# Optimization experiments

Measured on AMD Instinct MI355X. Metric: run time of the kernel, lower is better.

Reference implementation:

```python
import jax, jax.numpy as jnp
import numpy as np

B, S, E, H = 2, 2048, 1024, 16
D = E // H  # d_k = n_wires = 64


def setup_inputs() -> dict:
    key = jax.random.key(0)
    ks = jax.random.split(key, 6)
    x = jax.random.normal(ks[0], (B, S, E), dtype=jnp.float32)
    scale = 0.02
    Wq = jax.random.normal(ks[1], (E, E), dtype=jnp.float32) * scale
    Wk = jax.random.normal(ks[2], (E, E), dtype=jnp.float32) * scale
    Wv = jax.random.normal(ks[3], (E, E), dtype=jnp.float32) * scale
    Wc = jax.random.normal(ks[4], (E, E), dtype=jnp.float32) * scale
    bc = jnp.zeros((E,), dtype=jnp.float32)
    return {"x": x, "Wq": Wq, "Wk": Wk, "Wv": Wv, "Wc": Wc, "bc": bc}


def _split_heads(t):
    # [B,S,E] -> [B,H,S,D]
    return t.reshape(B, S, H, D).transpose(0, 2, 1, 3)


def _quantum(t):
    # RX(theta_i) per wire + CNOT ladder + per-wire PauliZ expectation:
    # <Z_j> = prod_{i<=j} cos(theta_i)  (closed form of the circuit)
    return jnp.cumprod(jnp.cos(t), axis=-1)


def reference(x, Wq, Wk, Wv, Wc, bc):
    q = _quantum(_split_heads(x @ Wq.T))  # [B,H,S,D]
    k = _quantum(_split_heads(x @ Wk.T))
    v = _quantum(_split_heads(x @ Wv.T))
    scores = jnp.einsum('bhsd,bhtd->bhst', q, k) / jnp.sqrt(jnp.float32(D))
    attn = jax.nn.softmax(scores, axis=-1)
    out = jnp.einsum('bhst,bhtd->bhsd', attn, v)  # [B,H,S,D]
    out = out.transpose(0, 2, 1, 3).reshape(B, S, E)
    return out @ Wc.T + bc
```

## Files before the change

### kernel.cpp

```cpp
#include <hip/hip_runtime.h>
#include <hip/hip_bf16.h>

constexpr int Bc = 2, Sc = 2048, Ec = 1024, Hc = 16, Dc = 64;
constexpr int Mrows = Bc * Sc;
constexpr int Kdim  = Ec;

#define QSCALE 0.18033688011112042f

typedef float  floatx4 __attribute__((ext_vector_type(4)));
typedef short  shortx8 __attribute__((ext_vector_type(8)));

__device__ __forceinline__ unsigned int pack2bf(float a, float b) {
    union { float f; unsigned int u; } ca, cb;
    ca.f = a; cb.f = b;
    return ((ca.u + 0x8000u) >> 16) | ((cb.u + 0x8000u) & 0xffff0000u);
}
__device__ inline float bf2f(unsigned short u) {
    union { unsigned int i; float f; } c; c.i = ((unsigned int)u) << 16; return c.f;
}
__device__ inline float exp2_fast(float x) {
#if __has_builtin(__builtin_amdgcn_exp2f)
    return __builtin_amdgcn_exp2f(x);
#else
    return __expf(x * 0.69314718056f);
#endif
}

__device__ __forceinline__ void gll16(const void* g, void* lds) {
    __builtin_amdgcn_global_load_lds(
        (const __attribute__((address_space(1))) void*)g,
        (__attribute__((address_space(3))) void*)lds, 16, 0, 0);
}

__global__ __launch_bounds__(256) void convert_all_kernel(
    const float* __restrict__ x,  const float* __restrict__ Wq,
    const float* __restrict__ Wk, const float* __restrict__ Wv,
    const float* __restrict__ Wc,
    unsigned short* __restrict__ xb,  unsigned short* __restrict__ Wqb,
    unsigned short* __restrict__ Wkb, unsigned short* __restrict__ Wvb,
    unsigned short* __restrict__ Wcb)
{
    const long t = (long)blockIdx.x * 256 + threadIdx.x;
    const long i = t * 4;
    const float* src; unsigned short* dst; long off;
    if (i < 4194304) { src = x; dst = xb; off = i; }
    else {
        long j = i - 4194304;
        int wsel = (int)(j >> 20);
        off = j & 1048575;
        src = (wsel == 0) ? Wq : (wsel == 1) ? Wk : (wsel == 2) ? Wv : Wc;
        dst = (wsel == 0) ? Wqb : (wsel == 1) ? Wkb : (wsel == 2) ? Wvb : Wcb;
    }
    float4 v = *(const float4*)(src + off);
    uint2 u;
    u.x = pack2bf(v.x, v.y);
    u.y = pack2bf(v.z, v.w);
    *(uint2*)(dst + off) = u;
}

__global__ __launch_bounds__(256) void proj_mfma_kernel(
    const unsigned short* __restrict__ Ab,
    const unsigned short* __restrict__ Wqb,
    const unsigned short* __restrict__ Wkb,
    const unsigned short* __restrict__ Wvb,
    unsigned short* __restrict__ oq,
    unsigned short* __restrict__ ok,
    unsigned short* __restrict__ ov)
{
    __shared__ __align__(16) char smem[33792];
    float (*Cs)[132] = (float(*)[132])smem;
    __shared__ float Sp[64][9];

    const int z = blockIdx.z;
    const unsigned short* Wb = (z == 0) ? Wqb : (z == 1) ? Wkb : Wvb;
    unsigned short* out      = (z == 0) ? oq  : (z == 1) ? ok  : ov;
    const int mode = (z == 2) ? 1 : 0;
    const float osc = (z == 0) ? QSCALE : 1.0f;

    const int tid = threadIdx.x;
    const int lane = tid & 63;
    const int w = tid >> 6, l15 = tid & 15, quad = (tid >> 4) & 3;
    const int wq = w >> 1, wn = w & 1;
    const int m0 = blockIdx.x * 128;
    const int n0 = blockIdx.y * 128;
    const int h0 = n0 >> 6;
    const int sw = l15 & 7;

    floatx4 acc[4][4];
    #pragma unroll
    for (int ms = 0; ms < 4; ++ms)
        #pragma unroll
        for (int ns = 0; ns < 4; ++ns)
            #pragma unroll
            for (int e = 0; e < 4; ++e) acc[ms][ns][e] = 0.0f;

    for (int k0 = 0; k0 < Kdim; k0 += 64) {
        #pragma unroll
        for (int j = 0; j < 4; ++j) {
            int idx = j * 64 + lane;
            int row = 32 * w + (idx >> 3);
            int cg  = ((idx & 7) ^ (idx >> 3)) & 7;
            gll16(Ab + (size_t)(m0 + row) * Kdim + k0 + cg * 8,
                  smem + 4096 * w + 1024 * j);
            gll16(Wb + (size_t)(n0 + row) * Kdim + k0 + cg * 8,
                  smem + 16384 + 4096 * w + 1024 * j);
        }
        __syncthreads();
        #pragma unroll
        for (int ks = 0; ks < 2; ++ks) {
            shortx8 af[4], bf[4];
            #pragma unroll
            for (int ms = 0; ms < 4; ++ms)
                af[ms] = *(shortx8*)(smem + (64 * wq + 16 * ms + l15) * 128
                                     + (((4 * ks + quad) ^ sw) << 4));
            #pragma unroll
            for (int ns = 0; ns < 4; ++ns)
                bf[ns] = *(shortx8*)(smem + 16384 + (64 * wn + 16 * ns + l15) * 128
                                     + (((4 * ks + quad) ^ sw) << 4));
            #pragma unroll
            for (int ms = 0; ms < 4; ++ms)
                #pragma unroll
                for (int ns = 0; ns < 4; ++ns)
                    acc[ms][ns] = __builtin_amdgcn_mfma_f32_16x16x32_bf16(
                        af[ms], bf[ns], acc[ms][ns], 0, 0, 0);
        }
        __syncthreads();
    }

    const int b = m0 >> 11;
    const int sbase = m0 & (Sc - 1);

    for (int pass = 0; pass < 2; ++pass) {
        if (wq == pass) {
            #pragma unroll
            for (int ms = 0; ms < 4; ++ms)
                #pragma unroll
                for (int ns = 0; ns < 4; ++ns)
                    #pragma unroll
                    for (int r = 0; r < 4; ++r)
                        Cs[16 * ms + 4 * quad + r][64 * wn + 16 * ns + l15] =
                            __cosf(acc[ms][ns][r]);
        }
        __syncthreads();
        #pragma unroll
        for (int t = tid; t < 512; t += 256) {
            int row = t >> 3, seg = t & 7;
            float pr = 1.0f;
            #pragma unroll
            for (int c = 0; c < 16; ++c) pr *= Cs[row][seg * 16 + c];
            Sp[row][seg] = pr;
        }
        __syncthreads();
        if (mode == 0) {
            #pragma unroll
            for (int t = tid; t < 512; t += 256) {
                int row = t >> 3, seg = t & 7;
                float p = 1.0f;
                for (int j = (seg & 4); j < seg; ++j) p *= Sp[row][j];
                unsigned int dw[8];
                #pragma unroll
                for (int c2 = 0; c2 < 8; ++c2) {
                    p *= Cs[row][seg * 16 + 2 * c2];     float a = p * osc;
                    p *= Cs[row][seg * 16 + 2 * c2 + 1]; float bb = p * osc;
                    dw[c2] = pack2bf(a, bb);
                }
                int h = h0 + (seg >> 2);
                int s = sbase + pass * 64 + row;
                size_t base = (((size_t)b * Hc + h) * Sc + s) * Dc + (seg & 3) * 16;
                *(uint4*)(out + base)     = *(uint4*)&dw[0];
                *(uint4*)(out + base + 8) = *(uint4*)&dw[4];
            }
            __syncthreads();
        } else {
            #pragma unroll
            for (int t = tid; t < 512; t += 256) {
                int row = t >> 3, seg = t & 7;
                float p = 1.0f;
                for (int j = (seg & 4); j < seg; ++j) p *= Sp[row][j];
                #pragma unroll
                for (int c = 0; c < 16; ++c) { p *= Cs[row][seg * 16 + c]; Cs[row][seg * 16 + c] = p; }
            }
            __syncthreads();
            #pragma unroll
            for (int t = tid; t < 512; t += 256) {
                int col = t >> 2, chunk = t & 3;
                int h = h0 + (col >> 6), d = col & 63;
                unsigned int dw[8];
                #pragma unroll
                for (int j2 = 0; j2 < 8; ++j2)
                    dw[j2] = pack2bf(Cs[chunk * 16 + 2 * j2][col],
                                     Cs[chunk * 16 + 2 * j2 + 1][col]);
                size_t base = (((size_t)b * Hc + h) * Dc + d) * Sc
                              + sbase + pass * 64 + chunk * 16;
                *(uint4*)(out + base)     = *(uint4*)&dw[0];
                *(uint4*)(out + base + 8) = *(uint4*)&dw[4];
            }
            __syncthreads();
        }
    }
}

__global__ __launch_bounds__(256) void attn_mfma_kernel(
    const unsigned short* __restrict__ qg,
    const unsigned short* __restrict__ kg,
    const unsigned short* __restrict__ vtg,
    unsigned short* __restrict__ o1,
    unsigned short* __restrict__ o2,
    float* __restrict__ lpart)
{
    __shared__ __align__(16) unsigned short Ks[2][32][64];
    __shared__ __align__(16) unsigned short VTs[2][64][32];
    __shared__ __align__(16) unsigned short Pq[64][72];

    const int tid  = threadIdx.x;
    const int lane = tid & 63;
    const int w    = tid >> 6;
    const int l15  = tid & 15;
    const int quad = (tid >> 4) & 3;
    const int qb   = blockIdx.x;
    const int half = blockIdx.y;
    const int bh   = blockIdx.z;
    const int sw   = l15 & 7;

    const unsigned short* qp = qg  + (size_t)bh * Sc * Dc;
    const unsigned short* kp = kg  + (size_t)bh * Sc * Dc;
    const unsigned short* vp = vtg + (size_t)bh * Dc * Sc;

    int qrow[2];
    shortx8 qf[2][2];
    #pragma unroll
    for (int qs = 0; qs < 2; ++qs) {
        qrow[qs] = qb * 128 + 32 * w + 16 * qs + l15;
        qf[qs][0] = *(const shortx8*)(qp + (size_t)qrow[qs] * Dc + 8 * quad);
        qf[qs][1] = *(const shortx8*)(qp + (size_t)qrow[qs] * Dc + 32 + 8 * quad);
    }

    floatx4 Oacc[2][4];
    #pragma unroll
    for (int qs = 0; qs < 2; ++qs)
        #pragma unroll
        for (int mt = 0; mt < 4; ++mt)
            #pragma unroll
            for (int e = 0; e < 4; ++e) Oacc[qs][mt][e] = 0.0f;
    float lsum[2] = {0.0f, 0.0f};

    const unsigned short* kgl = kp
        + (size_t)(half * 1024 + 8 * w + (lane >> 3)) * Dc
        + (((lane & 7) ^ ((lane >> 3) & 7)) * 8);
    const unsigned short* vgl = vp
        + (size_t)(16 * w + (lane >> 2)) * Sc + half * 1024 + (lane & 3) * 8;

    gll16(kgl, &Ks[0][8 * w][0]);
    gll16(vgl, &VTs[0][16 * w][0]);

    for (int it = 0; it < 32; ++it) {
        const int buf = it & 1;
        __syncthreads();
        if (it + 1 < 32) {
            const int nb = (it + 1) & 1;
            gll16(kgl + (size_t)(it + 1) * 32 * Dc, &Ks[nb][8 * w][0]);
            gll16(vgl + (it + 1) * 32,              &VTs[nb][16 * w][0]);
        }

        shortx8 kf[2][2], vf[4];
        #pragma unroll
        for (int ks = 0; ks < 2; ++ks)
            #pragma unroll
            for (int mtp = 0; mtp < 2; ++mtp)
                kf[ks][mtp] = *(shortx8*)&Ks[buf][16 * mtp + l15]
                                            [(((4 * ks + quad) ^ sw) & 7) * 8];
        #pragma unroll
        for (int mt = 0; mt < 4; ++mt)
            vf[mt] = *(shortx8*)&VTs[buf][16 * mt + l15][8 * quad];

        #pragma unroll
        for (int qs = 0; qs < 2; ++qs) {
            floatx4 st[2];
            #pragma unroll
            for (int mtp = 0; mtp < 2; ++mtp)
                #pragma unroll
                for (int e = 0; e < 4; ++e) st[mtp][e] = 0.0f;
            #pragma unroll
            for (int ks = 0; ks < 2; ++ks)
                #pragma unroll
                for (int mtp = 0; mtp < 2; ++mtp)
                    st[mtp] = __builtin_amdgcn_mfma_f32_16x16x32_bf16(
                        kf[ks][mtp], qf[qs][ks], st[mtp], 0, 0, 0);

            float rs = 0.0f;
            #pragma unroll
            for (int mtp = 0; mtp < 2; ++mtp) {
                float p0 = exp2_fast(st[mtp][0]);
                float p1 = exp2_fast(st[mtp][1]);
                float p2 = exp2_fast(st[mtp][2]);
                float p3 = exp2_fast(st[mtp][3]);
                rs += (p0 + p1) + (p2 + p3);
                uint2 u;
                u.x = pack2bf(p0, p1);
                u.y = pack2bf(p2, p3);
                *(uint2*)&Pq[16 * w + l15][16 * mtp + 4 * quad] = u;
            }
            lsum[qs] += rs;

            shortx8 pf = *(shortx8*)&Pq[16 * w + l15][8 * quad];
            #pragma unroll
            for (int mt = 0; mt < 4; ++mt)
                Oacc[qs][mt] = __builtin_amdgcn_mfma_f32_16x16x32_bf16(
                    vf[mt], pf, Oacc[qs][mt], 0, 0, 0);
        }
    }

    const int b = bh >> 4, hh = bh & 15;
    unsigned short* opart = half ? o2 : o1;
    float* lp = lpart + ((size_t)half * (Bc * Hc) + bh) * Sc;
    #pragma unroll
    for (int qs = 0; qs < 2; ++qs) {
        float l = lsum[qs];
        l += __shfl_xor(l, 16, 64);
        l += __shfl_xor(l, 32, 64);
        if (quad == 0) lp[qrow[qs]] = l;
        #pragma unroll
        for (int mt = 0; mt < 4; ++mt) {
            uint2 u;
            u.x = pack2bf(Oacc[qs][mt][0], Oacc[qs][mt][1]);
            u.y = pack2bf(Oacc[qs][mt][2], Oacc[qs][mt][3]);
            size_t base = ((size_t)b * Sc + qrow[qs]) * Ec + hh * 64 + 16 * mt + 4 * quad;
            *(uint2*)(opart + base) = u;
        }
    }
}

__global__ __launch_bounds__(256) void combine_kernel(
    unsigned short* __restrict__ o1,
    const unsigned short* __restrict__ o2,
    const float* __restrict__ lpart)
{
    const size_t t = (size_t)blockIdx.x * 256 + threadIdx.x;
    const size_t base = t * 8;
    const int e = (int)(base & (Ec - 1));
    const int h = e >> 6;
    const size_t bs = base >> 10;
    const int b = (int)(bs >> 11), s = (int)(bs & (Sc - 1));
    const int bh = b * Hc + h;
    const float l = lpart[(size_t)bh * Sc + s]
                  + lpart[(size_t)(Bc * Hc + bh) * Sc + s];
    const float inv = 1.0f / l;
    uint4 a = *(const uint4*)(o1 + base);
    uint4 c = *(const uint4*)(o2 + base);
    const unsigned short* ua = (const unsigned short*)&a;
    const unsigned short* uc = (const unsigned short*)&c;
    unsigned int dw[4];
    #pragma unroll
    for (int i = 0; i < 4; ++i)
        dw[i] = pack2bf((bf2f(ua[2 * i]) + bf2f(uc[2 * i])) * inv,
                        (bf2f(ua[2 * i + 1]) + bf2f(uc[2 * i + 1])) * inv);
    *(uint4*)(o1 + base) = *(uint4*)dw;
}

__global__ __launch_bounds__(256) void outproj_mfma_kernel(
    const unsigned short* __restrict__ Ab,
    const unsigned short* __restrict__ Wb,
    const float* __restrict__ bias,
    float* __restrict__ out)
{
    __shared__ __align__(16) char smem[24576];

    const int tid = threadIdx.x;
    const int lane = tid & 63;
    const int w = tid >> 6, l15 = tid & 15, quad = (tid >> 4) & 3;
    const int wq = w >> 1, wn = w & 1;
    const int m0 = blockIdx.x * 64;
    const int n0 = blockIdx.y * 128;
    const int sw = l15 & 7;

    floatx4 acc[2][4];
    #pragma unroll
    for (int ms = 0; ms < 2; ++ms)
        #pragma unroll
        for (int ns = 0; ns < 4; ++ns)
            #pragma unroll
            for (int e = 0; e < 4; ++e) acc[ms][ns][e] = 0.0f;

    for (int k0 = 0; k0 < Kdim; k0 += 64) {
        #pragma unroll
        for (int j = 0; j < 2; ++j) {
            int idx = j * 64 + lane;
            int row = 16 * w + (idx >> 3);
            int cg  = ((idx & 7) ^ (idx >> 3)) & 7;
            gll16(Ab + (size_t)(m0 + row) * Kdim + k0 + cg * 8,
                  smem + 2048 * w + 1024 * j);
        }
        #pragma unroll
        for (int j = 0; j < 4; ++j) {
            int idx = j * 64 + lane;
            int row = 32 * w + (idx >> 3);
            int cg  = ((idx & 7) ^ (idx >> 3)) & 7;
            gll16(Wb + (size_t)(n0 + row) * Kdim + k0 + cg * 8,
                  smem + 8192 + 4096 * w + 1024 * j);
        }
        __syncthreads();
        #pragma unroll
        for (int ks = 0; ks < 2; ++ks) {
            shortx8 af[2], bf[4];
            #pragma unroll
            for (int ms = 0; ms < 2; ++ms)
                af[ms] = *(shortx8*)(smem + (32 * wq + 16 * ms + l15) * 128
                                     + (((4 * ks + quad) ^ sw) << 4));
            #pragma unroll
            for (int ns = 0; ns < 4; ++ns)
                bf[ns] = *(shortx8*)(smem + 8192 + (64 * wn + 16 * ns + l15) * 128
                                     + (((4 * ks + quad) ^ sw) << 4));
            #pragma unroll
            for (int ms = 0; ms < 2; ++ms)
                #pragma unroll
                for (int ns = 0; ns < 4; ++ns)
                    acc[ms][ns] = __builtin_amdgcn_mfma_f32_16x16x32_bf16(
                        af[ms], bf[ns], acc[ms][ns], 0, 0, 0);
        }
        __syncthreads();
    }

    #pragma unroll
    for (int ns = 0; ns < 4; ++ns) {
        const float bv = bias[n0 + 64 * wn + 16 * ns + l15];
        #pragma unroll
        for (int ms = 0; ms < 2; ++ms)
            #pragma unroll
            for (int r = 0; r < 4; ++r) {
                int m = m0 + 32 * wq + 16 * ms + 4 * quad + r;
                out[(size_t)m * Kdim + n0 + 64 * wn + 16 * ns + l15] = acc[ms][ns][r] + bv;
            }
    }
}

extern "C" void kernel_launch(void* const* d_in, const int* in_sizes, int n_in,
                              void* d_out, int out_size, void* d_ws, size_t ws_size,
                              hipStream_t stream) {
    const float* x  = (const float*)d_in[0];
    const float* Wq = (const float*)d_in[1];
    const float* Wk = (const float*)d_in[2];
    const float* Wv = (const float*)d_in[3];
    const float* Wc = (const float*)d_in[4];
    const float* bc = (const float*)d_in[5];
    float* out = (float*)d_out;

    char* p = (char*)d_ws;
    unsigned short* xb   = (unsigned short*)(p);
    unsigned short* Wqb  = (unsigned short*)(p + (8u << 20));
    unsigned short* Wkb  = (unsigned short*)(p + (10u << 20));
    unsigned short* Wvb  = (unsigned short*)(p + (12u << 20));
    unsigned short* Wcb  = (unsigned short*)(p + (14u << 20));
    unsigned short* qb_  = (unsigned short*)(p + (16u << 20));
    unsigned short* kb_  = (unsigned short*)(p + (24u << 20));
    unsigned short* vtb  = (unsigned short*)(p + (32u << 20));
    unsigned short* attb = (unsigned short*)(p + (40u << 20));
    unsigned short* o2b  = xb;
    float*          lpart = (float*)(p + (8u << 20));

    hipLaunchKernelGGL(convert_all_kernel, dim3(8192), dim3(256), 0, stream,
                       x, Wq, Wk, Wv, Wc, xb, Wqb, Wkb, Wvb, Wcb);

    hipLaunchKernelGGL(proj_mfma_kernel, dim3(Mrows / 128, Ec / 128, 3), dim3(256), 0, stream,
                       xb, Wqb, Wkb, Wvb, qb_, kb_, vtb);

    hipLaunchKernelGGL(attn_mfma_kernel, dim3(Sc / 128, 2, Bc * Hc), dim3(256), 0, stream,
                       qb_, kb_, vtb, attb, o2b, lpart);

    hipLaunchKernelGGL(combine_kernel, dim3(Mrows * Ec / (256 * 8)), dim3(256), 0, stream,
                       attb, o2b, lpart);

    hipLaunchKernelGGL(outproj_mfma_kernel, dim3(Mrows / 64, Ec / 128), dim3(256), 0, stream,
                       attb, Wcb, bc, out);
}
```

Before: 214.2 us.

## Shuffle P fragments across lanes with bpermute and swizzle V^T shared tile

Replaces the shared-memory round-trip used to convert the exponentiated score fragment (MFMA output layout) into the B-operand layout with eight ds_bpermute lane shuffles plus selects. This drops the Pq LDS buffer and its write-then-read per query sub-tile. It also XOR-swizzles the column placement of the V^T tile in LDS, on both the global-to-LDS load and the fragment read, to reduce bank conflicts. The bpermutes still go through LDS hardware and add instructions, so the saving depends on whether the LDS traffic or the conflicts were actually the limit.

```diff
diff --git a/kernel.cpp b/kernel.cpp
--- a/kernel.cpp
+++ b/kernel.cpp
@@ -210,7 +210,6 @@
 {
     __shared__ __align__(16) unsigned short Ks[2][32][64];
     __shared__ __align__(16) unsigned short VTs[2][64][32];
-    __shared__ __align__(16) unsigned short Pq[64][72];
 
     const int tid  = threadIdx.x;
     const int lane = tid & 63;
@@ -244,11 +243,17 @@
             for (int e = 0; e < 4; ++e) Oacc[qs][mt][e] = 0.0f;
     float lsum[2] = {0.0f, 0.0f};
 
+    const int ixA = ((((quad & 1) << 5) | l15) << 2);
+    const int ixB = ixA + 64;
+
     const unsigned short* kgl = kp
         + (size_t)(half * 1024 + 8 * w + (lane >> 3)) * Dc
         + (((lane & 7) ^ ((lane >> 3) & 7)) * 8);
     const unsigned short* vgl = vp
-        + (size_t)(16 * w + (lane >> 2)) * Sc + half * 1024 + (lane & 3) * 8;
+        + (size_t)(16 * w + (lane >> 2)) * Sc + half * 1024
+        + (((lane & 3) ^ ((lane >> 3) & 3)) * 8);
+
+    const int vsw = (quad ^ ((l15 >> 1) & 3)) * 8;
 
     gll16(kgl, &Ks[0][8 * w][0]);
     gll16(vgl, &VTs[0][16 * w][0]);
@@ -271,7 +276,7 @@
                                             [(((4 * ks + quad) ^ sw) & 7) * 8];
         #pragma unroll
         for (int mt = 0; mt < 4; ++mt)
-            vf[mt] = *(shortx8*)&VTs[buf][16 * mt + l15][8 * quad];
+            vf[mt] = *(shortx8*)&VTs[buf][16 * mt + l15][vsw];
 
         #pragma unroll
         for (int qs = 0; qs < 2; ++qs) {
@@ -287,22 +292,32 @@
                     st[mtp] = __builtin_amdgcn_mfma_f32_16x16x32_bf16(
                         kf[ks][mtp], qf[qs][ks], st[mtp], 0, 0, 0);
 
-            float rs = 0.0f;
-            #pragma unroll
-            for (int mtp = 0; mtp < 2; ++mtp) {
-                float p0 = exp2_fast(st[mtp][0]);
-                float p1 = exp2_fast(st[mtp][1]);
-                float p2 = exp2_fast(st[mtp][2]);
-                float p3 = exp2_fast(st[mtp][3]);
-                rs += (p0 + p1) + (p2 + p3);
-                uint2 u;
-                u.x = pack2bf(p0, p1);
-                u.y = pack2bf(p2, p3);
-                *(uint2*)&Pq[16 * w + l15][16 * mtp + 4 * quad] = u;
-            }
-            lsum[qs] += rs;
-
-            shortx8 pf = *(shortx8*)&Pq[16 * w + l15][8 * quad];
+            float p00 = exp2_fast(st[0][0]), p01 = exp2_fast(st[0][1]);
+            float p02 = exp2_fast(st[0][2]), p03 = exp2_fast(st[0][3]);
+            float p10 = exp2_fast(st[1][0]), p11 = exp2_fast(st[1][1]);
+            float p12 = exp2_fast(st[1][2]), p13 = exp2_fast(st[1][3]);
+            lsum[qs] += ((p00 + p01) + (p02 + p03)) + ((p10 + p11) + (p12 + p13));
+            int u00 = (int)pack2bf(p00, p01);
+            int u01 = (int)pack2bf(p02, p03);
+            int u10 = (int)pack2bf(p10, p11);
+            int u11 = (int)pack2bf(p12, p13);
+
+            int a00 = __builtin_amdgcn_ds_bpermute(ixA, u00);
+            int a01 = __builtin_amdgcn_ds_bpermute(ixA, u01);
+            int a10 = __builtin_amdgcn_ds_bpermute(ixA, u10);
+            int a11 = __builtin_amdgcn_ds_bpermute(ixA, u11);
+            int b00 = __builtin_amdgcn_ds_bpermute(ixB, u00);
+            int b01 = __builtin_amdgcn_ds_bpermute(ixB, u01);
+            int b10 = __builtin_amdgcn_ds_bpermute(ixB, u10);
+            int b11 = __builtin_amdgcn_ds_bpermute(ixB, u11);
+            const bool hi = (quad >> 1) & 1;
+            int pfu[4];
+            pfu[0] = hi ? a10 : a00;
+            pfu[1] = hi ? a11 : a01;
+            pfu[2] = hi ? b10 : b00;
+            pfu[3] = hi ? b11 : b01;
+            shortx8 pf = *(shortx8*)pfu;
+
             #pragma unroll
             for (int mt = 0; mt < 4; ++mt)
                 Oacc[qs][mt] = __builtin_amdgcn_mfma_f32_16x16x32_bf16(
```

New measurement: 226.0 us. 5.5% more time.
